# Optimization experiments

Hardware: AMD Instinct MI355X
Metric: run time of the kernel (lower is better)

## Reference

```python
import jax, jax.numpy as jnp
import numpy as np


def setup_inputs() -> dict:
    key = jax.random.key(0)
    kx, kf = jax.random.split(key)
    x = jax.random.normal(kx, (4, 8192, 1024), dtype=jnp.float32)
    filt = jax.random.normal(kf, (2048,), dtype=jnp.float32)
    return {"x": x, "filt": filt}


def reference(x, filt):
    # x: (batch, seq, dim); filt: (filter_length,)
    batch, seq, dim = x.shape
    L = filt.shape[0]
    pad = seq + L - 1
    # long-sequence FFT branch (seq > 64)
    xt = jnp.swapaxes(x, 1, 2)                 # (b, d, s)
    fx = jnp.fft.rfft(xt, n=pad, axis=-1)      # (b, d, pad//2+1) complex
    ff = jnp.fft.rfft(filt[::-1], n=pad)       # (pad//2+1,) complex
    conv = jnp.fft.irfft(fx * ff, n=pad, axis=-1)  # (b, d, pad)
    conv = conv[:, :, L - 1:L - 1 + seq]       # valid region, length seq
    return jnp.swapaxes(conv, 1, 2)            # (b, s, d)
```

## Files before the change

### kernel.cpp

```cpp
#include <hip/hip_runtime.h>

typedef unsigned short u16;
typedef unsigned int   u32;

#define BATCH 4
#define SEQ   8192
#define DIM   1024
#define FL    2048
#define TROW  10240

#define BM 512
#define BN 64
#define BK 64
#define NSTAGE 40
#define WOFF 64
#define NW   2272
#define WIN_HI 2174

typedef float  f32x4  __attribute__((ext_vector_type(4)));
typedef __bf16 bf16x8 __attribute__((ext_vector_type(8)));
typedef short  s16x8  __attribute__((ext_vector_type(8)));

typedef const __attribute__((address_space(1))) void* gas_t;
typedef __attribute__((address_space(3))) void* las_t;

__device__ __forceinline__ u16 f2bf(float f) {
  u32 u = __float_as_uint(f);
  u += 0x7fffu + ((u >> 16) & 1u);
  return (u16)(u >> 16);
}

__global__ __launch_bounds__(256) void k_transpose(const float* __restrict__ x,
                                                   u16* __restrict__ xT) {
  __shared__ __align__(16) u16 sm[64 * 66];
  const int bid = blockIdx.x;
  const int tb = bid % (TROW / 64);
  const int db = (bid / (TROW / 64)) % (DIM / 64);
  const int b  = bid / ((TROW / 64) * (DIM / 64));
  const int t0 = tb * 64, d0 = db * 64;
  const int tid = threadIdx.x;

  const int c4 = tid & 15;
  const int lt = tid >> 4;
  const float* xb = x + (size_t)b * SEQ * DIM + d0 + c4 * 4;
  #pragma unroll
  for (int s = 0; s < 64; s += 16) {
    const int tl = lt + s;
    const int t = t0 + tl;
    float4 v = make_float4(0.f, 0.f, 0.f, 0.f);
    if (t < SEQ) v = *(const float4*)(xb + (size_t)t * DIM);
    u32 p0 = (u32)f2bf(v.x) | ((u32)f2bf(v.y) << 16);
    u32 p1 = (u32)f2bf(v.z) | ((u32)f2bf(v.w) << 16);
    u32* dst = (u32*)&sm[tl * 66 + c4 * 4];
    dst[0] = p0;
    dst[1] = p1;
  }
  __syncthreads();
  const int tp = tid & 31;
  const int dl = tid >> 5;
  u16* xo = xT + ((size_t)b * DIM + d0) * TROW + t0 + 2 * tp;
  #pragma unroll
  for (int s = 0; s < 64; s += 8) {
    const int d = dl + s;
    u32 v = (u32)sm[(2 * tp) * 66 + d] | ((u32)sm[(2 * tp + 1) * 66 + d] << 16);
    *(u32*)(xo + (size_t)d * TROW) = v;
  }
}

__global__ __launch_bounds__(256, 2) void k_conv(const u16* __restrict__ xT,
                                                 const float* __restrict__ filt,
                                                 float* __restrict__ out) {
  __shared__ __align__(16) u16 Wb[NW * 8];
  __shared__ __align__(16) u16 Xs[BN * BK];

  const int bid = blockIdx.x;
  const int tb = bid & 15;
  const int db = (bid >> 4) & 15;
  const int b  = bid >> 8;
  const int t0 = tb * BM;
  const int d0 = db * BN;

  const int tid  = threadIdx.x;
  const int wid  = tid >> 6;
  const int lane = tid & 63;
  const int quad = lane >> 4;
  const int lq   = lane & 15;
  const int Tw   = wid * 128;

  for (int w = tid; w < NW; w += 256) {
    const int base = w - WOFF;
    u32 pk[4];
    #pragma unroll
    for (int h = 0; h < 4; ++h) {
      const int i0 = base + 2 * h;
      const int i1 = i0 + 1;
      const float v0 = (i0 >= 0 && i0 < FL) ? filt[i0] : 0.f;
      const float v1 = (i1 >= 0 && i1 < FL) ? filt[i1] : 0.f;
      pk[h] = (u32)f2bf(v0) | ((u32)f2bf(v1) << 16);
    }
    u32* dst = (u32*)&Wb[w * 8];
    dst[0] = pk[0]; dst[1] = pk[1]; dst[2] = pk[2]; dst[3] = pk[3];
  }

  const u16* xrow = xT + ((size_t)b * DIM + d0) * TROW + t0;
  const int p0 = wid * 128 + lane;
  const int p1 = p0 + 64;
  const int ds0 = p0 >> 3, kc0 = (p0 & 7) ^ (ds0 & 7);
  const int ds1 = p1 >> 3, kc1 = (p1 & 7) ^ (ds1 & 7);
  const u16* gp0 = xrow + (size_t)ds0 * TROW + kc0 * 8;
  const u16* gp1 = xrow + (size_t)ds1 * TROW + kc1 * 8;
  u16* lds0 = &Xs[wid * 1024];
  u16* lds1 = lds0 + 512;

  f32x4 acc[8][4];
  const f32x4 fz = {0.f, 0.f, 0.f, 0.f};
  #pragma unroll
  for (int i = 0; i < 8; ++i)
    #pragma unroll
    for (int j = 0; j < 4; ++j) acc[i][j] = fz;

  const s16x8 sz = {0, 0, 0, 0, 0, 0, 0, 0};
  bf16x8 roll0 = __builtin_bit_cast(bf16x8, sz);
  bf16x8 roll1 = roll0, roll2 = roll0, roll3 = roll0, roll4 = roll0, roll5 = roll0;

  const int wconst = quad * 8 - Tw - lq + WOFF;
  const int kkLo = Tw - 31;
  const int kkHi = Tw + WIN_HI;

  for (int st = 0; st < NSTAGE; ++st) {
    const int kk0 = st * BK;
    __syncthreads();
    __builtin_amdgcn_global_load_lds((gas_t)(gp0 + kk0), (las_t)lds0, 16, 0, 0);
    __builtin_amdgcn_global_load_lds((gas_t)(gp1 + kk0), (las_t)lds1, 16, 0, 0);
    __syncthreads();
    #pragma unroll
    for (int half = 0; half < 2; ++half) {
      const int kk = kk0 + half * 32;
      if (kk >= kkLo && kk <= kkHi) {
        bf16x8 bfr[4];
        #pragma unroll
        for (int nt = 0; nt < 4; ++nt) {
          const int dl = nt * 16 + lq;
          const int kc = (half * 4 + quad) ^ (dl & 7);
          bfr[nt] = *(const bf16x8*)&Xs[(dl * 8 + kc) * 8];
        }
        const int w0 = kk + wconst;
        const bf16x8 a0 = *(const bf16x8*)&Wb[w0 * 8];
        const bf16x8 a1 = *(const bf16x8*)&Wb[(w0 - 16) * 8];
        #pragma unroll
        for (int nt = 0; nt < 4; ++nt) {
          acc[0][nt] = __builtin_amdgcn_mfma_f32_16x16x32_bf16(a0,    bfr[nt], acc[0][nt], 0, 0, 0);
          acc[1][nt] = __builtin_amdgcn_mfma_f32_16x16x32_bf16(a1,    bfr[nt], acc[1][nt], 0, 0, 0);
          acc[2][nt] = __builtin_amdgcn_mfma_f32_16x16x32_bf16(roll0, bfr[nt], acc[2][nt], 0, 0, 0);
          acc[3][nt] = __builtin_amdgcn_mfma_f32_16x16x32_bf16(roll1, bfr[nt], acc[3][nt], 0, 0, 0);
          acc[4][nt] = __builtin_amdgcn_mfma_f32_16x16x32_bf16(roll2, bfr[nt], acc[4][nt], 0, 0, 0);
          acc[5][nt] = __builtin_amdgcn_mfma_f32_16x16x32_bf16(roll3, bfr[nt], acc[5][nt], 0, 0, 0);
          acc[6][nt] = __builtin_amdgcn_mfma_f32_16x16x32_bf16(roll4, bfr[nt], acc[6][nt], 0, 0, 0);
          acc[7][nt] = __builtin_amdgcn_mfma_f32_16x16x32_bf16(roll5, bfr[nt], acc[7][nt], 0, 0, 0);
        }
        roll5 = roll3; roll4 = roll2; roll3 = roll1; roll2 = roll0;
        roll1 = a1; roll0 = a0;
      }
    }
  }

  float* ob = out + ((size_t)b * SEQ + t0 + Tw) * DIM + d0;
  #pragma unroll
  for (int mt = 0; mt < 8; ++mt) {
    #pragma unroll
    for (int nt = 0; nt < 4; ++nt) {
      #pragma unroll
      for (int r = 0; r < 4; ++r) {
        ob[(size_t)(mt * 16 + quad * 4 + r) * DIM + nt * 16 + lq] = acc[mt][nt][r];
      }
    }
  }
}

extern "C" void kernel_launch(void* const* d_in, const int* in_sizes, int n_in,
                              void* d_out, int out_size, void* d_ws, size_t ws_size,
                              hipStream_t stream) {
  const float* x    = (const float*)d_in[0];
  const float* filt = (const float*)d_in[1];
  float* out = (float*)d_out;
  u16* xT = (u16*)d_ws;
  (void)in_sizes; (void)n_in; (void)out_size; (void)ws_size;

  k_transpose<<<BATCH * (TROW / 64) * (DIM / 64), 256, 0, stream>>>(x, xT);
  k_conv<<<BATCH * 16 * 16, 256, 0, stream>>>(xT, filt, out);
}
```

Baseline: 347.6 us.

## Double-buffer conv LDS tiles with prefetch and vectorize transpose stores

The conv kernel now has two LDS buffers for the X tile. It issues the next stage's global-to-LDS loads before computing on the current buffer, which drops one barrier per stage and is meant to hide load latency behind the MFMA work. The transpose kernel now writes 16-byte vectors of eight bf16 values per thread instead of 4-byte stores. The overlap depends on where the compiler places its wait-counter checks around the async LDS loads, and the second buffer adds LDS use that could affect occupancy.

```diff
diff --git a/kernel.cpp b/kernel.cpp
--- a/kernel.cpp
+++ b/kernel.cpp
@@ -56,14 +56,19 @@
     dst[1] = p1;
   }
   __syncthreads();
-  const int tp = tid & 31;
-  const int dl = tid >> 5;
-  u16* xo = xT + ((size_t)b * DIM + d0) * TROW + t0 + 2 * tp;
-  #pragma unroll
-  for (int s = 0; s < 64; s += 8) {
-    const int d = dl + s;
-    u32 v = (u32)sm[(2 * tp) * 66 + d] | ((u32)sm[(2 * tp + 1) * 66 + d] << 16);
-    *(u32*)(xo + (size_t)d * TROW) = v;
+  const int q  = tid & 7;
+  const int dl = tid >> 3;
+  u16* xo = xT + ((size_t)b * DIM + d0) * TROW + t0 + 8 * q;
+  #pragma unroll
+  for (int s = 0; s < 2; ++s) {
+    const int d = dl + 32 * s;
+    u32 w[4];
+    #pragma unroll
+    for (int h = 0; h < 4; ++h) {
+      w[h] = (u32)sm[(8 * q + 2 * h) * 66 + d] |
+             ((u32)sm[(8 * q + 2 * h + 1) * 66 + d] << 16);
+    }
+    *(uint4*)(xo + (size_t)d * TROW) = *(const uint4*)w;
   }
 }
 
@@ -71,7 +76,7 @@
                                                  const float* __restrict__ filt,
                                                  float* __restrict__ out) {
   __shared__ __align__(16) u16 Wb[NW * 8];
-  __shared__ __align__(16) u16 Xs[BN * BK];
+  __shared__ __align__(16) u16 Xs[2][BN * BK];
 
   const int bid = blockIdx.x;
   const int tb = bid & 15;
@@ -109,8 +114,6 @@
   const int ds1 = p1 >> 3, kc1 = (p1 & 7) ^ (ds1 & 7);
   const u16* gp0 = xrow + (size_t)ds0 * TROW + kc0 * 8;
   const u16* gp1 = xrow + (size_t)ds1 * TROW + kc1 * 8;
-  u16* lds0 = &Xs[wid * 1024];
-  u16* lds1 = lds0 + 512;
 
   f32x4 acc[8][4];
   const f32x4 fz = {0.f, 0.f, 0.f, 0.f};
@@ -127,12 +130,22 @@
   const int kkLo = Tw - 31;
   const int kkHi = Tw + WIN_HI;
 
+  {
+    u16* nb = &Xs[0][wid * 1024];
+    __builtin_amdgcn_global_load_lds((gas_t)gp0, (las_t)nb, 16, 0, 0);
+    __builtin_amdgcn_global_load_lds((gas_t)gp1, (las_t)(nb + 512), 16, 0, 0);
+  }
+
   for (int st = 0; st < NSTAGE; ++st) {
+    __syncthreads();
+    if (st + 1 < NSTAGE) {
+      const int kkn = (st + 1) * BK;
+      u16* nb = &Xs[(st + 1) & 1][wid * 1024];
+      __builtin_amdgcn_global_load_lds((gas_t)(gp0 + kkn), (las_t)nb, 16, 0, 0);
+      __builtin_amdgcn_global_load_lds((gas_t)(gp1 + kkn), (las_t)(nb + 512), 16, 0, 0);
+    }
+    const u16* Xc = &Xs[st & 1][0];
     const int kk0 = st * BK;
-    __syncthreads();
-    __builtin_amdgcn_global_load_lds((gas_t)(gp0 + kk0), (las_t)lds0, 16, 0, 0);
-    __builtin_amdgcn_global_load_lds((gas_t)(gp1 + kk0), (las_t)lds1, 16, 0, 0);
-    __syncthreads();
     #pragma unroll
     for (int half = 0; half < 2; ++half) {
       const int kk = kk0 + half * 32;
@@ -142,7 +155,7 @@
         for (int nt = 0; nt < 4; ++nt) {
           const int dl = nt * 16 + lq;
           const int kc = (half * 4 + quad) ^ (dl & 7);
-          bfr[nt] = *(const bf16x8*)&Xs[(dl * 8 + kc) * 8];
+          bfr[nt] = *(const bf16x8*)&Xc[(dl * 8 + kc) * 8];
         }
         const int w0 = kk + wconst;
         const bf16x8 a0 = *(const bf16x8*)&Wb[w0 * 8];
```

Measured after the change: 345.0 us. About the same (-0.7%).
